# Kernel tuning notes

Hardware: AMD Instinct MI355X
Metric: run time of the kernel (lower is better)

Reference implementation:

```python
import jax, jax.numpy as jnp
import numpy as np

# Module config (matches init_kwargs attn_neighborhood_size=[7,7])
KH, KW = 7, 7
B, N_HEADS, HEIGHT, WIDTH, D = 2, 8, 48, 48, 64


def setup_inputs() -> dict:
    key = jax.random.key(0)
    x = jax.random.normal(key, (B, N_HEADS, HEIGHT * WIDTH, D), dtype=jnp.float32)
    return {"x": x, "height": HEIGHT, "width": WIDTH}


def reference(x, height, width):
    """LocalExpansion forward.

    The torch module runs conv2d with KH*KW one-hot impulse filters and
    padding='same'. Filter (i, j) with pad = (K-1)//2 produces
    out[y, x] = in[y + i - ph, x + j - pw] with zero fill at boundaries,
    i.e. a padded shifted gather (im2col/unfold). We implement that directly.

    x: [b, h, N, d] with N = height * width
    returns: [b, h, N, KH*KW, d]
    """
    b, h, n, d = x.shape
    img = x.reshape(b, h, height, width, d)  # [b, h, H, W, d]
    ph, pw = (KH - 1) // 2, (KW - 1) // 2  # 'same' padding for odd kernels
    xp = jnp.pad(img, ((0, 0), (0, 0), (ph, ph), (pw, pw), (0, 0)))
    # Filter index c = i * KW + j -> shifted slice (i outer, j inner),
    # matching the torch impulse-filter ordering.
    shifts = [
        xp[:, :, i:i + height, j:j + width, :]
        for i in range(KH) for j in range(KW)
    ]
    y = jnp.stack(shifts, axis=4)  # [b, h, H, W, K, d]
    return y.reshape(b, h, height * width, KH * KW, d)
```

## Files before the change

kernel.cpp:

```cpp
#include <hip/hip_runtime.h>


#define KH 7
#define KW 7
#define HEIGHT 48
#define WIDTH 48
#define DDIM 64
#define NPIX (HEIGHT * WIDTH)
#define KK (KH * KW)

__global__ __launch_bounds__(256) void local_expansion_kernel(
    const float* __restrict__ in, float* __restrict__ out) {
    int idx4 = blockIdx.x * 256 + threadIdx.x;

    int d4   = idx4 & 15;
    int rem  = idx4 >> 4;
    int c    = rem % KK;
    int rem2 = rem / KK;
    int n    = rem2 % NPIX;
    int bh   = rem2 / NPIX;

    int y = n / WIDTH;
    int x = n - y * WIDTH;
    int i = c / KW;
    int j = c - i * KW;

    int sy = y + i - (KH - 1) / 2;
    int sx = x + j - (KW - 1) / 2;

    float4 v = make_float4(0.f, 0.f, 0.f, 0.f);
    if ((unsigned)sy < (unsigned)HEIGHT && (unsigned)sx < (unsigned)WIDTH) {
        int in4 = (bh * NPIX + sy * WIDTH + sx) * (DDIM / 4) + d4;
        v = ((const float4*)in)[in4];
    }
    ((float4*)out)[idx4] = v;
}

extern "C" void kernel_launch(void* const* d_in, const int* in_sizes, int n_in,
                              void* d_out, int out_size, void* d_ws, size_t ws_size,
                              hipStream_t stream) {
    const float* x = (const float*)d_in[0];
    float* out = (float*)d_out;

    int total4 = out_size / 4;
    dim3 grid(total4 / 256);
    local_expansion_kernel<<<grid, 256, 0, stream>>>(x, out);
}
```

Baseline: 484.8 us.

## Stage input halo tile in LDS and write output contiguously per block

Each block now handles half an image row: it loads a 7-row halo tile of the input into shared memory, then writes all 49 neighborhood copies for its 24 pixels contiguously from LDS. This replaces 49-fold redundant global gathers and per-element div/mod by large constants. In exchange it uses about 53 KB of LDS per block, which limits occupancy, and adds a barrier between the load and store phases.

```diff
diff --git a/kernel.cpp b/kernel.cpp
--- a/kernel.cpp
+++ b/kernel.cpp
@@ -3,37 +3,55 @@
 
 #define KH 7
 #define KW 7
+#define PAD 3
 #define HEIGHT 48
 #define WIDTH 48
 #define DDIM 64
 #define NPIX (HEIGHT * WIDTH)
 #define KK (KH * KW)
+#define HALF 24
+#define LW (HALF + KW - 1)
+#define STAGE4 (KH * LW * (DDIM/4))
+#define OUT4 (HALF * KK * (DDIM/4))
 
 __global__ __launch_bounds__(256) void local_expansion_kernel(
     const float* __restrict__ in, float* __restrict__ out) {
-    int idx4 = blockIdx.x * 256 + threadIdx.x;
+    __shared__ float4 lds[STAGE4];
 
-    int d4   = idx4 & 15;
-    int rem  = idx4 >> 4;
-    int c    = rem % KK;
-    int rem2 = rem / KK;
-    int n    = rem2 % NPIX;
-    int bh   = rem2 / NPIX;
+    int blk = blockIdx.x;
+    int h   = blk & 1;
+    int yb  = blk >> 1;
+    int y0  = yb % HEIGHT;
+    int bh  = yb / HEIGHT;
+    int x0  = h * HALF;
 
-    int y = n / WIDTH;
-    int x = n - y * WIDTH;
-    int i = c / KW;
-    int j = c - i * KW;
+    const float4* in4 = (const float4*)in;
 
-    int sy = y + i - (KH - 1) / 2;
-    int sx = x + j - (KW - 1) / 2;
+    for (int s = threadIdx.x; s < STAGE4; s += 256) {
+        int r   = s / (LW * 16);
+        int rem = s - r * (LW * 16);
+        int p   = rem >> 4;
+        int d4  = rem & 15;
+        int gy  = y0 - PAD + r;
+        int gx  = x0 - PAD + p;
+        float4 v = make_float4(0.f, 0.f, 0.f, 0.f);
+        if ((unsigned)gy < (unsigned)HEIGHT && (unsigned)gx < (unsigned)WIDTH)
+            v = in4[(bh * NPIX + gy * WIDTH + gx) * 16 + d4];
+        lds[s] = v;
+    }
+    __syncthreads();
 
-    float4 v = make_float4(0.f, 0.f, 0.f, 0.f);
-    if ((unsigned)sy < (unsigned)HEIGHT && (unsigned)sx < (unsigned)WIDTH) {
-        int in4 = (bh * NPIX + sy * WIDTH + sx) * (DDIM / 4) + d4;
-        v = ((const float4*)in)[in4];
+    int obase = (bh * NPIX + y0 * WIDTH + x0) * (KK * 16);
+    float4* o4 = (float4*)out + obase;
+    for (int s = threadIdx.x; s < OUT4; s += 256) {
+        int q   = s / (KK * 16);
+        int rem = s - q * (KK * 16);
+        int c   = rem >> 4;
+        int d4  = rem & 15;
+        int i   = c / KW;
+        int j   = c - i * KW;
+        o4[s] = lds[(i * LW + q + j) * 16 + d4];
     }
-    ((float4*)out)[idx4] = v;
 }
 
 extern "C" void kernel_launch(void* const* d_in, const int* in_sizes, int n_in,
@@ -42,7 +60,6 @@
     const float* x = (const float*)d_in[0];
     float* out = (float*)d_out;
 
-    int total4 = out_size / 4;
-    dim3 grid(total4 / 256);
-    local_expansion_kernel<<<grid, 256, 0, stream>>>(x, out);
+    int blocks = 16 * HEIGHT * 2;
+    local_expansion_kernel<<<dim3(blocks), 256, 0, stream>>>(x, out);
 }
```

Result: faster. 464.3 us (-4.2%).
